# Kernel optimization log

Hardware: AMD Instinct MI355X
Metric: run time of the kernel (lower is better)

## Reference

```python
import jax, jax.numpy as jnp
import numpy as np

N_NODES = 100000
N_EDGES = 1600000
DIM = 64

def setup_inputs() -> dict:
    key = jax.random.key(0)
    k1, k2, k3 = jax.random.split(key, 3)
    x = jax.random.normal(k1, (N_NODES, DIM), dtype=jnp.float32)
    edge_index = jax.random.randint(k2, (2, N_EDGES), 0, N_NODES, dtype=jnp.int64)
    edge_weight = jax.random.uniform(k3, (N_EDGES,), dtype=jnp.float32)
    return {"x": x, "edge_index": edge_index, "edge_weight": edge_weight}

def reference(x, edge_index, edge_weight):
    # out[row] += x[col] * edge_weight  (edge-weighted gather + scatter-add)
    row, col = edge_index[0], edge_index[1]
    messages = x[col] * edge_weight[:, None]            # [E, dim]
    out = jax.ops.segment_sum(messages, row, num_segments=x.shape[0])  # [N, dim]
    return out
```

## Files before the change

kernel.cpp:

```cpp
#include <hip/hip_runtime.h>
#include <hip/hip_fp16.h>
#include <stdint.h>


typedef unsigned long long ull;
typedef int   v4i __attribute__((ext_vector_type(4)));
typedef float v4f __attribute__((ext_vector_type(4)));
typedef unsigned char  uchar;
typedef unsigned short ushortt;

#define RB      64
#define CAP     1280
#define CHUNK   4096
#define EPT     8
#define SLOTS   48
#define BPAD    16
#define OVF_CAP 65536
#define NBP     2048

__device__ __forceinline__ unsigned short f2bf(float f) {
    union { float f; unsigned int u; } c;
    c.f = f;
    unsigned int lsb = (c.u >> 16) & 1u;
    c.u += 0x7fffu + lsb;
    return (unsigned short)(c.u >> 16);
}
__device__ __forceinline__ float bf2f(unsigned short u) {
    union { unsigned int u; float f; } c;
    c.u = ((unsigned int)u) << 16;
    return c.f;
}
__device__ __forceinline__ unsigned pack_cw(int col, float w) {
    unsigned hb = __half_as_ushort(__float2half(w));
    return (((unsigned)col) << 15) | (hb >> 1);
}
__device__ __forceinline__ float unpack_w(unsigned v) {
    return __half2float(__ushort_as_half((unsigned short)((v & 0x7fffu) << 1)));
}

__global__ __launch_bounds__(512) void prep(
    const int* __restrict__ ei, const float* __restrict__ ew,
    int* __restrict__ bcnt, unsigned* __restrict__ s4g,
    uchar* __restrict__ srg,
    int* __restrict__ ovf_cnt, int3* __restrict__ ovf, int E, int NB,
    int nbin, const float* __restrict__ x, unsigned short* __restrict__ xb,
    int n4)
{
    __shared__ int      hist[NBP];
    __shared__ int      lstart[NBP];
    __shared__ int      gbase[NBP];
    __shared__ int      wsum[8];
    __shared__ unsigned s4_l[CHUNK];
    __shared__ uchar    sr_l[CHUNK];
    __shared__ ushortt  bk_l[CHUNK];
    int t = threadIdx.x;

    if ((int)blockIdx.x >= nbin) {
        int i0 = ((int)blockIdx.x - nbin) * 4096 + t;
#pragma unroll
        for (int k = 0; k < 8; ++k) {
            int i = i0 + k * 512;
            if (i < n4) {
                v4f v = ((const v4f*)x)[i];
                ushort4 o;
                o.x = f2bf(v.x); o.y = f2bf(v.y);
                o.z = f2bf(v.z); o.w = f2bf(v.w);
                ((ushort4*)xb)[i] = o;
            }
        }
        return;
    }

    for (int i = t; i < NBP; i += 512) hist[i] = 0;
    __syncthreads();

    int e0   = blockIdx.x * CHUNK;
    int nval = E - e0; if (nval > CHUNK) nval = CHUNK;
    bool al4 = ((E & 3) == 0);

    int      rk[EPT];
    unsigned br[EPT];
    unsigned p4[EPT];
    bool     vd[EPT];
#pragma unroll
    for (int j = 0; j < EPT / 4; ++j) {
        int eb = e0 + (j * 512 + t) * 4;
        v4i r4, c4; v4f w4;
        if (al4 && eb + 3 < E) {
            r4 = *(const v4i*)(ei + eb);
            c4 = *(const v4i*)(ei + E + eb);
            w4 = *(const v4f*)(ew + eb);
        } else {
#pragma unroll
            for (int u = 0; u < 4; ++u) {
                int e = eb + u;
                r4[u] = e < E ? ei[e] : 0;
                c4[u] = e < E ? ei[E + e] : 0;
                w4[u] = e < E ? ew[e] : 0.f;
            }
        }
#pragma unroll
        for (int u = 0; u < 4; ++u) {
            int idx = j * 4 + u;
            int e = eb + u;
            vd[idx] = e < E;
            int bkt = r4[u] >> 6;
            rk[idx] = vd[idx] ? atomicAdd(&hist[bkt], 1) : 0;
            br[idx] = (unsigned)((bkt << 6) | (r4[u] & (RB - 1)));
            p4[idx] = pack_cw(c4[u], w4[u]);
        }
    }
    __syncthreads();

    for (int i = t; i < NB; i += 512) {
        int h = hist[i];
        gbase[i] = h ? atomicAdd(&bcnt[i * BPAD], h) : 0;
    }
    {
        int h0 = hist[4 * t],     h1 = hist[4 * t + 1];
        int h2 = hist[4 * t + 2], h3 = hist[4 * t + 3];
        int ps = h0 + h1 + h2 + h3;
        int lane = t & 63, wid = t >> 6;
        int s = ps;
#pragma unroll
        for (int off = 1; off < 64; off <<= 1) {
            int o = __shfl_up(s, off);
            if (lane >= off) s += o;
        }
        if (lane == 63) wsum[wid] = s;
        __syncthreads();
        if (t < 8) {
            int v = wsum[t];
            int s2 = v;
#pragma unroll
            for (int off = 1; off < 8; off <<= 1) {
                int o = __shfl_up(s2, off);
                if (t >= off) s2 += o;
            }
            wsum[t] = s2 - v;
        }
        __syncthreads();
        int excl = s - ps + wsum[wid];
        lstart[4 * t]     = excl;
        lstart[4 * t + 1] = excl + h0;
        lstart[4 * t + 2] = excl + h0 + h1;
        lstart[4 * t + 3] = excl + h0 + h1 + h2;
    }
    __syncthreads();

#pragma unroll
    for (int j = 0; j < EPT; ++j) {
        if (!vd[j]) continue;
        int bkt = (int)(br[j] >> 6);
        int lp  = lstart[bkt] + rk[j];
        s4_l[lp] = p4[j];
        sr_l[lp] = (uchar)(br[j] & (RB - 1));
        bk_l[lp] = (ushortt)bkt;
    }
    __syncthreads();

    for (int i = t; i < nval; i += 512) {
        int bkt = (int)bk_l[i];
        int loc = gbase[bkt] + (i - lstart[bkt]);
        unsigned p = s4_l[i];
        if (loc < CAP) {
            size_t gp = (size_t)bkt * CAP + loc;
            s4g[gp] = p;
            srg[gp] = sr_l[i];
        } else {
            int o = atomicAdd(ovf_cnt, 1);
            if (o < OVF_CAP)
                ovf[o] = make_int3(bkt * RB + (int)sr_l[i],
                                   (int)(p >> 15),
                                   __float_as_int(unpack_w(p)));
        }
    }
}

template <bool BF>
__global__ __launch_bounds__(256, 8) void bucket_acc(
    const void* __restrict__ xv, const unsigned* __restrict__ s4g,
    const uchar* __restrict__ srg,
    const int* __restrict__ bcnt, float* __restrict__ out,
    int* __restrict__ ovf_cnt, int3* __restrict__ ovf, int N)
{
    __shared__ int      cur[RB];
    __shared__ unsigned tile[RB * SLOTS];
    int t = threadIdx.x;
    int g = blockIdx.x;
    if (t < RB) cur[t] = 0;
    __syncthreads();

    int c = bcnt[g * BPAD];
    if (c > CAP) c = CAP;
    const unsigned* b4 = s4g + (size_t)g * CAP;
    const uchar*    br = srg + (size_t)g * CAP;

    for (int i = t; i < c; i += 256) {
        unsigned p4 = b4[i];
        int rl = br[i];
        int pos = atomicAdd(&cur[rl], 1);
        if (pos < SLOTS) {
            tile[rl * SLOTS + pos] = p4;
        } else {
            int o = atomicAdd(ovf_cnt, 1);
            if (o < OVF_CAP)
                ovf[o] = make_int3(g * RB + rl, (int)(p4 >> 15),
                                   __float_as_int(unpack_w(p4)));
        }
    }
    __syncthreads();

    int wid  = t >> 6;
    int lane = t & 63;
    const unsigned short* xh = (const unsigned short*)xv;
    const float*          xf = (const float*)xv;

    for (int k = 0; k < 16; ++k) {
        int r   = wid * 16 + k;
        int row = g * RB + r;
        if (row >= N) break;
        int cc = cur[r];
        if (cc > SLOTS) cc = SLOTS;
        const unsigned* tb = &tile[r * SLOTS];

        float acc = 0.0f;
        int p = 0;
        for (; p + 8 <= cc; p += 8) {
            unsigned a[8]; float xr[8];
#pragma unroll
            for (int i = 0; i < 8; ++i) a[i] = tb[p + i];
#pragma unroll
            for (int i = 0; i < 8; ++i) {
                size_t off = (((size_t)(a[i] >> 15)) << 6) + lane;
                xr[i] = BF ? bf2f(xh[off]) : xf[off];
            }
#pragma unroll
            for (int i = 0; i < 8; ++i)
                acc = fmaf(xr[i], unpack_w(a[i]), acc);
        }
        if (p < cc) {
            unsigned a[8]; float xr[8], w[8];
#pragma unroll
            for (int i = 0; i < 8; ++i) {
                int q = p + i;
                bool valid = q < cc;
                if (!valid) q = cc - 1;
                a[i] = tb[q];
                w[i] = valid ? unpack_w(a[i]) : 0.0f;
            }
#pragma unroll
            for (int i = 0; i < 8; ++i) {
                size_t off = (((size_t)(a[i] >> 15)) << 6) + lane;
                xr[i] = BF ? bf2f(xh[off]) : xf[off];
            }
#pragma unroll
            for (int i = 0; i < 8; ++i) acc = fmaf(xr[i], w[i], acc);
        }
        __builtin_nontemporal_store(acc, out + (((size_t)row) << 6) + lane);
    }
}

template <bool BF>
__global__ __launch_bounds__(256) void ovf_apply(
    const void* __restrict__ xv, const int* __restrict__ ovf_cnt,
    const int3* __restrict__ ovf, float* __restrict__ out)
{
    int n = *ovf_cnt;
    if (n > OVF_CAP) n = OVF_CAP;
    int wid  = (blockIdx.x * 256 + threadIdx.x) >> 6;
    int lane = threadIdx.x & 63;
    int nw   = gridDim.x * 4;
    for (int o = wid; o < n; o += nw) {
        int3 tt = ovf[o];
        float w = __int_as_float(tt.z);
        size_t off = (((size_t)tt.y) << 6) + lane;
        float x = BF ? bf2f(((const unsigned short*)xv)[off])
                     : ((const float*)xv)[off];
        atomicAdd(&out[(((size_t)tt.x) << 6) + lane], x * w);
    }
}

__global__ __launch_bounds__(256) void scatter_edges(
    const float* __restrict__ x, const int* __restrict__ ei,
    const float* __restrict__ ew, float* __restrict__ out, int E)
{
    long long idx = (long long)blockIdx.x * 256 + threadIdx.x;
    int e = (int)(idx >> 4);
    if (e >= E) return;
    int j = (int)(idx & 15);
    int row = ei[e];
    int col = ei[E + e];
    float w = ew[e];
    v4f v = *(const v4f*)(x + (((size_t)col) << 6) + (j << 2));
    float* op = out + (((size_t)row) << 6) + (j << 2);
    atomicAdd(op + 0, v.x * w);
    atomicAdd(op + 1, v.y * w);
    atomicAdd(op + 2, v.z * w);
    atomicAdd(op + 3, v.w * w);
}

extern "C" void kernel_launch(void* const* d_in, const int* in_sizes, int n_in,
                              void* d_out, int out_size, void* d_ws, size_t ws_size,
                              hipStream_t stream) {
    const float* x  = (const float*)d_in[0];
    const int*   ei = (const int*)d_in[1];
    const float* ew = (const float*)d_in[2];
    float*       out = (float*)d_out;

    int E = in_sizes[2];
    int N = out_size / 64;
    int NB = (N + RB - 1) / RB;

    size_t ovf_base  = (size_t)NB * BPAD + 2;
    size_t xb_base   = (ovf_base + 3 * (size_t)OVF_CAP + 3) & ~(size_t)3;
    size_t xb_ints   = (size_t)N * 32;
    size_t s4_ints   = (size_t)NB * CAP;
    size_t sr_ints   = ((size_t)NB * CAP + 3) / 4;

    size_t s4_base_bf  = xb_base + xb_ints;
    size_t sr_base_bf  = s4_base_bf + s4_ints;
    size_t need_bf     = (sr_base_bf + sr_ints) * 4;

    size_t s4_base_f   = xb_base;
    size_t sr_base_f   = s4_base_f + s4_ints;
    size_t need_f      = (sr_base_f + sr_ints) * 4;

    int nbin  = (E + CHUNK - 1) / CHUNK;
    int n4    = (N * 64) / 4;
    int nconv = (n4 + 4095) / 4096;

    if ((ws_size >= need_bf || ws_size >= need_f) && N <= (1 << 17)) {
        bool use_bf = ws_size >= need_bf;
        int* w32 = (int*)d_ws;
        int* bcnt = w32;
        int* ovf_cnt = w32 + NB * BPAD;
        int3* ovf = (int3*)(w32 + ovf_base);
        unsigned short* xb = (unsigned short*)(w32 + xb_base);
        unsigned* s4g = (unsigned*)(w32 + (use_bf ? s4_base_bf : s4_base_f));
        uchar*    srg = (uchar*)(w32 + (use_bf ? sr_base_bf : sr_base_f));

        (void)hipMemsetAsync(w32, 0, ((size_t)NB * BPAD + 2) * sizeof(int),
                             stream);

        if (use_bf) {
            prep<<<nbin + nconv, 512, 0, stream>>>(
                ei, ew, bcnt, s4g, srg, ovf_cnt, ovf, E, NB, nbin, x, xb, n4);
            bucket_acc<true><<<NB, 256, 0, stream>>>(
                xb, s4g, srg, bcnt, out, ovf_cnt, ovf, N);
            ovf_apply<true><<<64, 256, 0, stream>>>(xb, ovf_cnt, ovf, out);
        } else {
            prep<<<nbin, 512, 0, stream>>>(
                ei, ew, bcnt, s4g, srg, ovf_cnt, ovf, E, NB, nbin, x, xb, 0);
            bucket_acc<false><<<NB, 256, 0, stream>>>(
                x, s4g, srg, bcnt, out, ovf_cnt, ovf, N);
            ovf_apply<false><<<64, 256, 0, stream>>>(x, ovf_cnt, ovf, out);
        }
    } else {
        (void)hipMemsetAsync(out, 0, (size_t)out_size * sizeof(float), stream);
        long long threads = (long long)E * 16;
        scatter_edges<<<(int)((threads + 255) / 256), 256, 0, stream>>>(
            x, ei, ew, out, E);
    }
}
```

Before: 180.6 us.

## Replace single-pass 2048-bucket binning with two-pass radix binning via superbuckets

Edge binning now runs in two passes. First, edges are scattered into 32 superbuckets of 4096 rows using 64-bit packed records. A new bin2 kernel then re-sorts each superbucket into 64 fine buckets of 64 rows. This avoids the large shared histogram, the scan over 2048 bins and the scattered global writes across ~1600 buckets in the first pass. In exchange it adds an extra kernel launch and a full extra read/write pass over 8-byte records, and it drops the fp32 fallback path.

```diff
diff --git a/kernel.cpp b/kernel.cpp
--- a/kernel.cpp
+++ b/kernel.cpp
@@ -7,7 +7,6 @@
 typedef int   v4i __attribute__((ext_vector_type(4)));
 typedef float v4f __attribute__((ext_vector_type(4)));
 typedef unsigned char  uchar;
-typedef unsigned short ushortt;
 
 #define RB      64
 #define CAP     1280
@@ -16,7 +15,8 @@
 #define SLOTS   48
 #define BPAD    16
 #define OVF_CAP 65536
-#define NBP     2048
+#define NSBP    32
+#define SBROWS  4096
 
 __device__ __forceinline__ unsigned short f2bf(float f) {
     union { float f; unsigned int u; } c;
@@ -30,29 +30,20 @@
     c.u = ((unsigned int)u) << 16;
     return c.f;
 }
-__device__ __forceinline__ unsigned pack_cw(int col, float w) {
-    unsigned hb = __half_as_ushort(__float2half(w));
-    return (((unsigned)col) << 15) | (hb >> 1);
-}
 __device__ __forceinline__ float unpack_w(unsigned v) {
     return __half2float(__ushort_as_half((unsigned short)((v & 0x7fffu) << 1)));
 }
 
 __global__ __launch_bounds__(512) void prep(
     const int* __restrict__ ei, const float* __restrict__ ew,
-    int* __restrict__ bcnt, unsigned* __restrict__ s4g,
-    uchar* __restrict__ srg,
-    int* __restrict__ ovf_cnt, int3* __restrict__ ovf, int E, int NB,
-    int nbin, const float* __restrict__ x, unsigned short* __restrict__ xb,
-    int n4)
+    int* __restrict__ bcnt1, ull* __restrict__ seg1, int cap1,
+    int* __restrict__ ovf_cnt, int3* __restrict__ ovf, int E, int nbin,
+    const float* __restrict__ x, unsigned short* __restrict__ xb, int n4)
 {
-    __shared__ int      hist[NBP];
-    __shared__ int      lstart[NBP];
-    __shared__ int      gbase[NBP];
-    __shared__ int      wsum[8];
-    __shared__ unsigned s4_l[CHUNK];
-    __shared__ uchar    sr_l[CHUNK];
-    __shared__ ushortt  bk_l[CHUNK];
+    __shared__ int hist[NSBP];
+    __shared__ int lstart[NSBP];
+    __shared__ int gbase[NSBP];
+    __shared__ ull sorted[CHUNK];
     int t = threadIdx.x;
 
     if ((int)blockIdx.x >= nbin) {
@@ -71,17 +62,17 @@
         return;
     }
 
-    for (int i = t; i < NBP; i += 512) hist[i] = 0;
+    if (t < NSBP) hist[t] = 0;
     __syncthreads();
 
     int e0   = blockIdx.x * CHUNK;
     int nval = E - e0; if (nval > CHUNK) nval = CHUNK;
     bool al4 = ((E & 3) == 0);
 
-    int      rk[EPT];
-    unsigned br[EPT];
-    unsigned p4[EPT];
-    bool     vd[EPT];
+    int   rk[EPT];
+    uchar sb[EPT];
+    ull   cw[EPT];
+    bool  vd[EPT];
 #pragma unroll
     for (int j = 0; j < EPT / 4; ++j) {
         int eb = e0 + (j * 512 + t) * 4;
@@ -104,83 +95,140 @@
             int idx = j * 4 + u;
             int e = eb + u;
             vd[idx] = e < E;
-            int bkt = r4[u] >> 6;
-            rk[idx] = vd[idx] ? atomicAdd(&hist[bkt], 1) : 0;
-            br[idx] = (unsigned)((bkt << 6) | (r4[u] & (RB - 1)));
-            p4[idx] = pack_cw(c4[u], w4[u]);
-        }
-    }
-    __syncthreads();
-
-    for (int i = t; i < NB; i += 512) {
-        int h = hist[i];
-        gbase[i] = h ? atomicAdd(&bcnt[i * BPAD], h) : 0;
-    }
-    {
-        int h0 = hist[4 * t],     h1 = hist[4 * t + 1];
-        int h2 = hist[4 * t + 2], h3 = hist[4 * t + 3];
-        int ps = h0 + h1 + h2 + h3;
-        int lane = t & 63, wid = t >> 6;
-        int s = ps;
-#pragma unroll
-        for (int off = 1; off < 64; off <<= 1) {
+            int b = r4[u] >> 12;
+            rk[idx] = vd[idx] ? atomicAdd(&hist[b], 1) : 0;
+            sb[idx] = (uchar)b;
+            unsigned hw = __half_as_ushort(__float2half(w4[u]));
+            cw[idx] = ((ull)hw << 48) | ((ull)(unsigned)r4[u] << 24) |
+                      (ull)(unsigned)c4[u];
+        }
+    }
+    __syncthreads();
+
+    if (t < 32) {
+        int h = hist[t];
+        gbase[t] = h ? atomicAdd(&bcnt1[t * BPAD], h) : 0;
+        int s = h;
+#pragma unroll
+        for (int off = 1; off < 32; off <<= 1) {
             int o = __shfl_up(s, off);
-            if (lane >= off) s += o;
-        }
-        if (lane == 63) wsum[wid] = s;
-        __syncthreads();
-        if (t < 8) {
-            int v = wsum[t];
-            int s2 = v;
-#pragma unroll
-            for (int off = 1; off < 8; off <<= 1) {
-                int o = __shfl_up(s2, off);
-                if (t >= off) s2 += o;
-            }
-            wsum[t] = s2 - v;
-        }
-        __syncthreads();
-        int excl = s - ps + wsum[wid];
-        lstart[4 * t]     = excl;
-        lstart[4 * t + 1] = excl + h0;
-        lstart[4 * t + 2] = excl + h0 + h1;
-        lstart[4 * t + 3] = excl + h0 + h1 + h2;
+            if (t >= off) s += o;
+        }
+        lstart[t] = s - h;
     }
     __syncthreads();
 
 #pragma unroll
     for (int j = 0; j < EPT; ++j) {
         if (!vd[j]) continue;
-        int bkt = (int)(br[j] >> 6);
-        int lp  = lstart[bkt] + rk[j];
-        s4_l[lp] = p4[j];
-        sr_l[lp] = (uchar)(br[j] & (RB - 1));
-        bk_l[lp] = (ushortt)bkt;
+        sorted[lstart[sb[j]] + rk[j]] = cw[j];
     }
     __syncthreads();
 
     for (int i = t; i < nval; i += 512) {
-        int bkt = (int)bk_l[i];
-        int loc = gbase[bkt] + (i - lstart[bkt]);
-        unsigned p = s4_l[i];
-        if (loc < CAP) {
-            size_t gp = (size_t)bkt * CAP + loc;
-            s4g[gp] = p;
-            srg[gp] = sr_l[i];
+        ull e = sorted[i];
+        int b = (int)((e >> 24) & 0x1FFFF) >> 12;
+        int loc = gbase[b] + (i - lstart[b]);
+        if (loc < cap1) {
+            seg1[(size_t)b * cap1 + loc] = e;
         } else {
             int o = atomicAdd(ovf_cnt, 1);
             if (o < OVF_CAP)
-                ovf[o] = make_int3(bkt * RB + (int)sr_l[i],
-                                   (int)(p >> 15),
-                                   __float_as_int(unpack_w(p)));
+                ovf[o] = make_int3((int)((e >> 24) & 0x1FFFF),
+                                   (int)(e & 0x1FFFF),
+                                   __float_as_int(__half2float(
+                                       __ushort_as_half((unsigned short)(e >> 48)))));
+        }
+    }
+}
+
+__global__ __launch_bounds__(512) void bin2(
+    const ull* __restrict__ seg1, int cap1, const int* __restrict__ bcnt1,
+    int* __restrict__ bcnt, ull* __restrict__ seg2,
+    int* __restrict__ ovf_cnt, int3* __restrict__ ovf, int chpersb)
+{
+    __shared__ int hist[64];
+    __shared__ int lstart[64];
+    __shared__ int gbase[64];
+    __shared__ ull sorted[CHUNK];
+    int t  = threadIdx.x;
+    int sb = blockIdx.x / chpersb;
+    int ch = blockIdx.x % chpersb;
+
+    int cnt1 = bcnt1[sb * BPAD];
+    if (cnt1 > cap1) cnt1 = cap1;
+    int s0 = ch * CHUNK;
+    int nval = cnt1 - s0;
+    if (nval <= 0) return;
+    if (nval > CHUNK) nval = CHUNK;
+
+    if (t < 64) hist[t] = 0;
+    __syncthreads();
+
+    const ull* base = seg1 + (size_t)sb * cap1 + s0;
+
+    int   rk[EPT];
+    uchar fb[EPT];
+    ull   cw[EPT];
+    bool  vd[EPT];
+#pragma unroll
+    for (int j = 0; j < EPT; ++j) {
+        int i = t + j * 512;
+        vd[j] = i < nval;
+        ull e = vd[j] ? base[i] : 0;
+        int row = (int)((e >> 24) & 0x1FFFF);
+        int f = (row >> 6) & 63;
+        rk[j] = vd[j] ? atomicAdd(&hist[f], 1) : 0;
+        fb[j] = (uchar)f;
+        cw[j] = e;
+    }
+    __syncthreads();
+
+    if (t < 64) {
+        int h = hist[t];
+        int fbg = sb * 64 + t;
+        gbase[t] = h ? atomicAdd(&bcnt[fbg * BPAD], h) : 0;
+        int s = h;
+#pragma unroll
+        for (int off = 1; off < 64; off <<= 1) {
+            int o = __shfl_up(s, off);
+            if (t >= off) s += o;
+        }
+        lstart[t] = s - h;
+    }
+    __syncthreads();
+
+#pragma unroll
+    for (int j = 0; j < EPT; ++j) {
+        if (!vd[j]) continue;
+        sorted[lstart[fb[j]] + rk[j]] = cw[j];
+    }
+    __syncthreads();
+
+    for (int i = t; i < nval; i += 512) {
+        ull e = sorted[i];
+        int row = (int)((e >> 24) & 0x1FFFF);
+        int f = (row >> 6) & 63;
+        int loc = gbase[f] + (i - lstart[f]);
+        int fbg = sb * 64 + f;
+        if (loc < CAP) {
+            ull hw = (e >> 48) & 0xFFFF;
+            seg2[(size_t)fbg * CAP + loc] =
+                (hw << 32) | ((ull)(unsigned)(row & 63) << 17) |
+                (e & 0x1FFFF);
+        } else {
+            int o = atomicAdd(ovf_cnt, 1);
+            if (o < OVF_CAP)
+                ovf[o] = make_int3(row, (int)(e & 0x1FFFF),
+                                   __float_as_int(__half2float(
+                                       __ushort_as_half((unsigned short)(e >> 48)))));
         }
     }
 }
 
 template <bool BF>
 __global__ __launch_bounds__(256, 8) void bucket_acc(
-    const void* __restrict__ xv, const unsigned* __restrict__ s4g,
-    const uchar* __restrict__ srg,
+    const void* __restrict__ xv, const ull* __restrict__ seg2,
     const int* __restrict__ bcnt, float* __restrict__ out,
     int* __restrict__ ovf_cnt, int3* __restrict__ ovf, int N)
 {
@@ -193,12 +241,13 @@
 
     int c = bcnt[g * BPAD];
     if (c > CAP) c = CAP;
-    const unsigned* b4 = s4g + (size_t)g * CAP;
-    const uchar*    br = srg + (size_t)g * CAP;
+    const ull* b8 = seg2 + (size_t)g * CAP;
 
     for (int i = t; i < c; i += 256) {
-        unsigned p4 = b4[i];
-        int rl = br[i];
+        ull e = b8[i];
+        int rl = (int)((e >> 17) & 63);
+        unsigned p4 = ((unsigned)(e & 0x1FFFF) << 15) |
+                      ((unsigned)(e >> 33) & 0x7FFF);
         int pos = atomicAdd(&cur[rl], 1);
         if (pos < SLOTS) {
             tile[rl * SLOTS + pos] = p4;
@@ -310,52 +359,46 @@
 
     int E = in_sizes[2];
     int N = out_size / 64;
-    int NB = (N + RB - 1) / RB;
-
-    size_t ovf_base  = (size_t)NB * BPAD + 2;
+    int NB  = (N + RB - 1) / RB;
+    int NSB = (N + SBROWS - 1) / SBROWS;
+
+    long long mean1 = (long long)E * SBROWS / (N > 0 ? N : 1);
+    int cap1 = (int)(mean1 + mean1 / 20 + CHUNK);
+    cap1 = (cap1 + 1023) & ~1023;
+    int chpersb = (cap1 + CHUNK - 1) / CHUNK;
+
+    size_t bcnt_base = (size_t)NSBP * BPAD;
+    size_t ovfc_base = bcnt_base + (size_t)NB * BPAD;
+    size_t ovf_base  = (ovfc_base + 1 + 3) & ~(size_t)3;
     size_t xb_base   = (ovf_base + 3 * (size_t)OVF_CAP + 3) & ~(size_t)3;
-    size_t xb_ints   = (size_t)N * 32;
-    size_t s4_ints   = (size_t)NB * CAP;
-    size_t sr_ints   = ((size_t)NB * CAP + 3) / 4;
-
-    size_t s4_base_bf  = xb_base + xb_ints;
-    size_t sr_base_bf  = s4_base_bf + s4_ints;
-    size_t need_bf     = (sr_base_bf + sr_ints) * 4;
-
-    size_t s4_base_f   = xb_base;
-    size_t sr_base_f   = s4_base_f + s4_ints;
-    size_t need_f      = (sr_base_f + sr_ints) * 4;
+    size_t seg1_base = (xb_base + (size_t)N * 32 + 1) & ~(size_t)1;
+    size_t seg2_base = seg1_base + (size_t)NSB * cap1 * 2;
+    size_t need      = (seg2_base + (size_t)NB * CAP * 2) * 4;
 
     int nbin  = (E + CHUNK - 1) / CHUNK;
     int n4    = (N * 64) / 4;
-    int nconv = (n4 + 4095) / 4096;
-
-    if ((ws_size >= need_bf || ws_size >= need_f) && N <= (1 << 17)) {
-        bool use_bf = ws_size >= need_bf;
+    int nconv = (n4 + CHUNK - 1) / CHUNK;
+
+    if (ws_size >= need && N <= (1 << 17)) {
         int* w32 = (int*)d_ws;
-        int* bcnt = w32;
-        int* ovf_cnt = w32 + NB * BPAD;
-        int3* ovf = (int3*)(w32 + ovf_base);
+        int* bcnt1   = w32;
+        int* bcnt    = w32 + bcnt_base;
+        int* ovf_cnt = w32 + ovfc_base;
+        int3* ovf    = (int3*)(w32 + ovf_base);
         unsigned short* xb = (unsigned short*)(w32 + xb_base);
-        unsigned* s4g = (unsigned*)(w32 + (use_bf ? s4_base_bf : s4_base_f));
-        uchar*    srg = (uchar*)(w32 + (use_bf ? sr_base_bf : sr_base_f));
-
-        (void)hipMemsetAsync(w32, 0, ((size_t)NB * BPAD + 2) * sizeof(int),
-                             stream);
-
-        if (use_bf) {
-            prep<<<nbin + nconv, 512, 0, stream>>>(
-                ei, ew, bcnt, s4g, srg, ovf_cnt, ovf, E, NB, nbin, x, xb, n4);
-            bucket_acc<true><<<NB, 256, 0, stream>>>(
-                xb, s4g, srg, bcnt, out, ovf_cnt, ovf, N);
-            ovf_apply<true><<<64, 256, 0, stream>>>(xb, ovf_cnt, ovf, out);
-        } else {
-            prep<<<nbin, 512, 0, stream>>>(
-                ei, ew, bcnt, s4g, srg, ovf_cnt, ovf, E, NB, nbin, x, xb, 0);
-            bucket_acc<false><<<NB, 256, 0, stream>>>(
-                x, s4g, srg, bcnt, out, ovf_cnt, ovf, N);
-            ovf_apply<false><<<64, 256, 0, stream>>>(x, ovf_cnt, ovf, out);
-        }
+        ull* seg1 = (ull*)(w32 + seg1_base);
+        ull* seg2 = (ull*)(w32 + seg2_base);
+
+        (void)hipMemsetAsync(w32, 0,
+            (bcnt_base + (size_t)NB * BPAD + 2) * sizeof(int), stream);
+
+        prep<<<nbin + nconv, 512, 0, stream>>>(
+            ei, ew, bcnt1, seg1, cap1, ovf_cnt, ovf, E, nbin, x, xb, n4);
+        bin2<<<NSB * chpersb, 512, 0, stream>>>(
+            seg1, cap1, bcnt1, bcnt, seg2, ovf_cnt, ovf, chpersb);
+        bucket_acc<true><<<NB, 256, 0, stream>>>(
+            xb, seg2, bcnt, out, ovf_cnt, ovf, N);
+        ovf_apply<true><<<64, 256, 0, stream>>>(xb, ovf_cnt, ovf, out);
     } else {
         (void)hipMemsetAsync(out, 0, (size_t)out_size * sizeof(float), stream);
         long long threads = (long long)E * 16;
```

Measured after the change: 163.6 us. 1.1x faster.
